# Optimization experiments

Measured on AMD Instinct MI355X. Metric: run time of the kernel, lower is better.

## Reference

```python
import jax, jax.numpy as jnp
import numpy as np

N_NODES = 100000
N_EDGES = 1600000
N_LABEL = 100000
IN_C, H1, H2, OUT_C = 128, 128, 64, 64
MLP_H = 64


def _glorot(key, shape):
    fan_in, fan_out = shape[0], shape[1]
    s = jnp.sqrt(6.0 / (fan_in + fan_out))
    return jax.random.uniform(key, shape, jnp.float32, -s, s)


def setup_inputs() -> dict:
    key = jax.random.key(0)
    ks = jax.random.split(key, 12)
    x = jax.random.normal(ks[0], (N_NODES, IN_C), jnp.float32)
    edge_index = jax.random.randint(ks[1], (2, N_EDGES), 0, N_NODES, jnp.int64)
    edge_label_index = jax.random.randint(ks[2], (2, N_LABEL), 0, N_NODES, jnp.int64)
    return {
        "x": x,
        "edge_index": edge_index,
        "edge_label_index": edge_label_index,
        "W1": _glorot(ks[3], (IN_C, H1)), "b1": jnp.zeros((H1,), jnp.float32),
        "W2": _glorot(ks[4], (H1, H2)), "b2": jnp.zeros((H2,), jnp.float32),
        "W3": _glorot(ks[5], (H2, OUT_C)), "b3": jnp.zeros((OUT_C,), jnp.float32),
        "Wl1": _glorot(ks[6], (2 * OUT_C, MLP_H)), "bl1": jnp.zeros((MLP_H,), jnp.float32),
        "Wl2": _glorot(ks[7], (MLP_H, 1)), "bl2": jnp.zeros((1,), jnp.float32),
    }


def reference(x, edge_index, edge_label_index, W1, b1, W2, b2, W3, b3, Wl1, bl1, Wl2, bl2):
    n = x.shape[0]
    # GCNConv: add self-loops once; symmetric deg^{-1/2} normalization.
    loops = jnp.arange(n, dtype=edge_index.dtype)
    src = jnp.concatenate([edge_index[0], loops])  # [E+N]
    dst = jnp.concatenate([edge_index[1], loops])
    deg = jax.ops.segment_sum(jnp.ones_like(dst, dtype=x.dtype), dst, num_segments=n)
    deg_isqrt = jnp.where(deg > 0, jax.lax.rsqrt(jnp.maximum(deg, 1e-12)), 0.0)
    norm = deg_isqrt[src] * deg_isqrt[dst]  # [E+N]

    def conv(h, W, b):
        m = (h @ W)[src] * norm[:, None]          # gather + scale per edge
        return jax.ops.segment_sum(m, dst, num_segments=n) + b  # scatter-add

    z = jax.nn.relu(conv(x, W1, b1))   # dropout is identity at eval
    z = jax.nn.relu(conv(z, W2, b2))
    z = conv(z, W3, b3)                # [N, OUT_C]

    s, d = edge_label_index[0], edge_label_index[1]
    pairs = jnp.concatenate([z[s], z[d]], axis=1)  # [E_label, 2*OUT_C]
    h = jax.nn.relu(pairs @ Wl1 + bl1)
    logits = (h @ Wl2 + bl2)[:, 0]
    return logits
```

## Files before the change

### kernel.cpp

```cpp
#include <hip/hip_runtime.h>


typedef _Float16 half8 __attribute__((ext_vector_type(8)));
typedef float floatx4 __attribute__((ext_vector_type(4)));

#define EPB 8
#define CHUNK (256 * EPB)


__global__ __launch_bounds__(256) void k_hist_wsplit(
    const int* __restrict__ ei, int E, int n, int* __restrict__ cnt,
    unsigned short* __restrict__ rank,
    const float* __restrict__ W1, _Float16* __restrict__ Wf1,
    const float* __restrict__ W2, _Float16* __restrict__ Wf2,
    const float* __restrict__ W3, _Float16* __restrict__ Wf3, int HB) {
  int b = blockIdx.x;
  if (b < HB) {
    int role = b & 7, chunk = b >> 3;
    int ns = (n + 7) / 8;
    int lo = role * ns, hi = min(n, lo + ns);
    int e0 = chunk * CHUNK + threadIdx.x;
#pragma unroll
    for (int q = 0; q < EPB; ++q) {
      int e = e0 + q * 256;
      if (e < E) {
        int d = __builtin_nontemporal_load(ei + E + e);
        if (d >= lo && d < hi) {
          int r = atomicAdd(&cnt[d], 1);
          rank[e] = (unsigned short)r;
        }
      }
    }
    return;
  }
  b -= HB;
  const float* W;
  _Float16* Wf;
  int KC, lc;
  if (b < 64)      { W = W1; Wf = Wf1; KC = 16384; lc = 7; }
  else if (b < 96) { b -= 64; W = W2; Wf = Wf2; KC = 8192; lc = 6; }
  else             { b -= 96; W = W3; Wf = Wf3; KC = 4096; lc = 6; }
  int t = b * 256 + threadIdx.x;
  if (t >= KC) return;
  int C = 1 << lc;
  int c = t & (C - 1), k = t >> lc;
  float a = W[t];
  _Float16 h = (_Float16)a;
  _Float16 l = (_Float16)(a - (float)h);
  int ks = k >> 5, ct = c >> 4;
  int lane = ((k & 31) >> 3) * 16 + (c & 15);
  int j = k & 7;
  int base = ((ks * (C >> 4) + ct) * 2) * 512 + lane * 8 + j;
  Wf[base] = h;
  Wf[base + 512] = l;
}


__global__ void k_scan1(const int* __restrict__ cnt, int* __restrict__ bsum, int n) {
  __shared__ int s[256];
  int i = blockIdx.x * 256 + threadIdx.x;
  int t = threadIdx.x;
  s[t] = (i < n) ? cnt[i] : 0;
  __syncthreads();
  for (int d = 128; d > 0; d >>= 1) {
    if (t < d) s[t] += s[t + d];
    __syncthreads();
  }
  if (t == 0) bsum[blockIdx.x] = s[0];
}

__global__ void k_scan23(const int* __restrict__ cnt, const int* __restrict__ bsum,
                         int nb, int* __restrict__ rs, float* __restrict__ isq,
                         int n) {
  __shared__ int s[256];
  __shared__ int off;
  int t = threadIdx.x;
  int b = blockIdx.x;
  int acc = 0;
  for (int j = t; j < b; j += 256) acc += bsum[j];
  s[t] = acc;
  __syncthreads();
  for (int d = 128; d > 0; d >>= 1) {
    if (t < d) s[t] += s[t + d];
    __syncthreads();
  }
  if (t == 0) off = s[0];
  __syncthreads();
  int blockoff = off;
  __syncthreads();
  int i = b * 256 + t;
  int v = (i < n) ? cnt[i] : 0;
  s[t] = v;
  __syncthreads();
  for (int d = 1; d < 256; d <<= 1) {
    int u = (t >= d) ? s[t - d] : 0;
    __syncthreads();
    s[t] += u;
    __syncthreads();
  }
  if (i < n) {
    int excl = blockoff + s[t] - v;
    rs[i] = excl;
    isq[i] = rsqrtf((float)(v + 1));
    if (i == n - 1) rs[n] = excl + v;
  }
}


__global__ __launch_bounds__(256) void k_fill(const int* __restrict__ ei, int E,
                                              int n, const int* __restrict__ rs,
                                              const unsigned short* __restrict__ rank,
                                              int* __restrict__ csr) {
  int role = blockIdx.x & 7, chunk = blockIdx.x >> 3;
  int ns = (n + 7) / 8;
  int lo = role * ns, hi = min(n, lo + ns);
  int e0 = chunk * CHUNK + threadIdx.x;
#pragma unroll
  for (int q = 0; q < EPB; ++q) {
    int e = e0 + q * 256;
    if (e < E) {
      int d = __builtin_nontemporal_load(ei + E + e);
      if (d >= lo && d < hi) {
        int s = __builtin_nontemporal_load(ei + e);
        int r = __builtin_nontemporal_load(rank + e);
        csr[rs[d] + r] = s;
      }
    }
  }
}


template <int K, int C>
__global__ __launch_bounds__(256) void k_gemm_mfma(const float* __restrict__ A,
                                                   const _Float16* __restrict__ Wf,
                                                   const float* __restrict__ isq,
                                                   _Float16* __restrict__ out, int n) {
  constexpr int NK = K / 32, NCT = C / 16;
  constexpr int WH = NK * NCT * 2 * 512;
  __shared__ __align__(16) _Float16 Wl[WH];
  int t = threadIdx.x;
  for (int i = t; i < WH / 8; i += 256)
    ((uint4*)Wl)[i] = ((const uint4*)Wf)[i];
  __syncthreads();

  int lane = t & 63, w = t >> 6;
  int rowbase = blockIdx.x * 128 + w * 32;
  int ar0 = rowbase + (lane & 15);
  int kg = (lane >> 4) * 8;

  floatx4 acc[2][NCT];
#pragma unroll
  for (int g = 0; g < 2; ++g)
#pragma unroll
    for (int ct = 0; ct < NCT; ++ct) acc[g][ct] = (floatx4){0.f, 0.f, 0.f, 0.f};

  for (int ks = 0; ks < NK; ++ks) {
    half8 ah[2], al[2];
#pragma unroll
    for (int g = 0; g < 2; ++g) {
      int row = ar0 + g * 16;
      if (row > n - 1) row = n - 1;
      const float* ap = A + (size_t)row * K + ks * 32 + kg;
      float4 u0 = ((const float4*)ap)[0];
      float4 u1 = ((const float4*)ap)[1];
      float av[8] = {u0.x, u0.y, u0.z, u0.w, u1.x, u1.y, u1.z, u1.w};
#pragma unroll
      for (int q = 0; q < 8; ++q) {
        _Float16 h = (_Float16)av[q];
        ah[g][q] = h;
        al[g][q] = (_Float16)(av[q] - (float)h);
      }
    }
#pragma unroll
    for (int ct = 0; ct < NCT; ++ct) {
      const _Float16* bp = &Wl[((ks * NCT + ct) * 2) * 512 + lane * 8];
      half8 bh = *(const half8*)bp;
      half8 bl = *(const half8*)(bp + 512);
#pragma unroll
      for (int g = 0; g < 2; ++g) {
        acc[g][ct] = __builtin_amdgcn_mfma_f32_16x16x32_f16(ah[g], bh, acc[g][ct], 0, 0, 0);
        acc[g][ct] = __builtin_amdgcn_mfma_f32_16x16x32_f16(ah[g], bl, acc[g][ct], 0, 0, 0);
        acc[g][ct] = __builtin_amdgcn_mfma_f32_16x16x32_f16(al[g], bh, acc[g][ct], 0, 0, 0);
      }
    }
  }
  int drbase = rowbase + (lane >> 4) * 4;
  int col = lane & 15;
#pragma unroll
  for (int g = 0; g < 2; ++g)
#pragma unroll
    for (int r = 0; r < 4; ++r) {
      int row = drbase + g * 16 + r;
      if (row < n) {
        float s = isq[row];
#pragma unroll
        for (int ct = 0; ct < NCT; ++ct)
          out[(size_t)row * C + ct * 16 + col] = (_Float16)(acc[g][ct][r] * s);
      }
    }
}


template <bool RELU>
__global__ __launch_bounds__(256) void k_agg128(const _Float16* __restrict__ xs,
                                                const int* __restrict__ rs,
                                                const int* __restrict__ csr,
                                                const float* __restrict__ isq,
                                                const float* __restrict__ bias,
                                                float* __restrict__ out, int n) {
  int gw = (int)((blockIdx.x * blockDim.x + threadIdx.x) >> 6);
  int lane = threadIdx.x & 63;
  if (gw >= n) return;
  int e0 = rs[gw], e1 = rs[gw + 1];
  int qtr = lane >> 4, sub = lane & 15;
  float acc[8] = {};
  int e = e0 + qtr;
  for (; e + 12 < e1; e += 16) {
    int a = __builtin_nontemporal_load(csr + e);
    int b = __builtin_nontemporal_load(csr + e + 4);
    int c = __builtin_nontemporal_load(csr + e + 8);
    int d = __builtin_nontemporal_load(csr + e + 12);
    half8 va = *(const half8*)&xs[(size_t)a * 128 + 8 * sub];
    half8 vb = *(const half8*)&xs[(size_t)b * 128 + 8 * sub];
    half8 vc = *(const half8*)&xs[(size_t)c * 128 + 8 * sub];
    half8 vd = *(const half8*)&xs[(size_t)d * 128 + 8 * sub];
#pragma unroll
    for (int j = 0; j < 8; ++j)
      acc[j] += (float)va[j] + (float)vb[j] + (float)vc[j] + (float)vd[j];
  }
  for (; e < e1; e += 4) {
    int a = __builtin_nontemporal_load(csr + e);
    half8 va = *(const half8*)&xs[(size_t)a * 128 + 8 * sub];
#pragma unroll
    for (int j = 0; j < 8; ++j) acc[j] += (float)va[j];
  }
#pragma unroll
  for (int j = 0; j < 8; ++j) {
    acc[j] += __shfl_xor(acc[j], 32, 64);
    acc[j] += __shfl_xor(acc[j], 16, 64);
  }
  if (qtr == 0) {
    float qi = isq[gw];
    half8 self = *(const half8*)&xs[(size_t)gw * 128 + 8 * sub];
#pragma unroll
    for (int j = 0; j < 8; ++j) {
      float r = qi * (acc[j] + (float)self[j]) + bias[8 * sub + j];
      if (RELU) r = fmaxf(r, 0.f);
      out[(size_t)gw * 128 + 8 * sub + j] = r;
    }
  }
}


template <bool RELU>
__global__ __launch_bounds__(256) void k_agg64(const _Float16* __restrict__ xs,
                                               const int* __restrict__ rs,
                                               const int* __restrict__ csr,
                                               const float* __restrict__ isq,
                                               const float* __restrict__ bias,
                                               float* __restrict__ out, int n) {
  int gw = (int)((blockIdx.x * blockDim.x + threadIdx.x) >> 6);
  int lane = threadIdx.x & 63;
  if (gw >= n) return;
  int e0 = rs[gw], e1 = rs[gw + 1];
  int oct = lane >> 3, sub = lane & 7;
  float acc[8] = {};
  int e = e0 + oct;
  for (; e + 8 < e1; e += 16) {
    int a = __builtin_nontemporal_load(csr + e);
    int b = __builtin_nontemporal_load(csr + e + 8);
    half8 va = *(const half8*)&xs[(size_t)a * 64 + 8 * sub];
    half8 vb = *(const half8*)&xs[(size_t)b * 64 + 8 * sub];
#pragma unroll
    for (int j = 0; j < 8; ++j) acc[j] += (float)va[j] + (float)vb[j];
  }
  for (; e < e1; e += 8) {
    int a = __builtin_nontemporal_load(csr + e);
    half8 va = *(const half8*)&xs[(size_t)a * 64 + 8 * sub];
#pragma unroll
    for (int j = 0; j < 8; ++j) acc[j] += (float)va[j];
  }
#pragma unroll
  for (int j = 0; j < 8; ++j) {
    acc[j] += __shfl_xor(acc[j], 32, 64);
    acc[j] += __shfl_xor(acc[j], 16, 64);
    acc[j] += __shfl_xor(acc[j], 8, 64);
  }
  if (oct == 0) {
    float qi = isq[gw];
    half8 self = *(const half8*)&xs[(size_t)gw * 64 + 8 * sub];
#pragma unroll
    for (int j = 0; j < 8; ++j) {
      float r = qi * (acc[j] + (float)self[j]) + bias[8 * sub + j];
      if (RELU) r = fmaxf(r, 0.f);
      out[(size_t)gw * 64 + 8 * sub + j] = r;
    }
  }
}


__global__ __launch_bounds__(256) void k_mlp(const float* __restrict__ z,
                                             const int* __restrict__ eli, int nlab,
                                             const float* __restrict__ Wl1,
                                             const float* __restrict__ bl1,
                                             const float* __restrict__ Wl2,
                                             const float* __restrict__ bl2,
                                             float* __restrict__ out) {
  constexpr int K = 128, TM = 4, LDA = K + 4;
  __shared__ float Wl[K * 64];
  __shared__ float Al[64 * LDA];
  int t = threadIdx.x;
  for (int i = t; i < K * 64 / 4; i += 256)
    ((float4*)Wl)[i] = ((const float4*)Wl1)[i];
  int rowbase = blockIdx.x * 64;
  {
    int r = t >> 2, p = t & 3;
    int row = rowbase + r;
    int idx = 0;
    if (row < nlab) idx = (p < 2) ? eli[row] : eli[nlab + row];
    const float4* src = (const float4*)(z + (size_t)idx * 64);
    int srcq = (p & 1) * 8;
    int dst = r * LDA + (p >= 2 ? 64 : 0) + (p & 1) * 32;
#pragma unroll
    for (int q = 0; q < 8; ++q)
      *(float4*)&Al[dst + 4 * q] = src[srcq + q];
  }
  __syncthreads();
  int tx = t & 15, ty = t >> 4;
  float acc[TM][4] = {};
  for (int k = 0; k < K; ++k) {
    float a[TM];
#pragma unroll
    for (int i = 0; i < TM; ++i) a[i] = Al[(ty * TM + i) * LDA + k];
    float4 w = *(const float4*)&Wl[k * 64 + tx * 4];
#pragma unroll
    for (int i = 0; i < TM; ++i) {
      acc[i][0] += a[i] * w.x;
      acc[i][1] += a[i] * w.y;
      acc[i][2] += a[i] * w.z;
      acc[i][3] += a[i] * w.w;
    }
  }
  float4 b1v = *(const float4*)&bl1[tx * 4];
  float4 w2v = *(const float4*)&Wl2[tx * 4];
  float bias2 = bl2[0];
  float part[TM];
#pragma unroll
  for (int i = 0; i < TM; ++i) {
    float h0 = fmaxf(acc[i][0] + b1v.x, 0.f);
    float h1 = fmaxf(acc[i][1] + b1v.y, 0.f);
    float h2 = fmaxf(acc[i][2] + b1v.z, 0.f);
    float h3 = fmaxf(acc[i][3] + b1v.w, 0.f);
    part[i] = h0 * w2v.x + h1 * w2v.y + h2 * w2v.z + h3 * w2v.w;
  }
#pragma unroll
  for (int i = 0; i < TM; ++i) {
#pragma unroll
    for (int m = 1; m < 16; m <<= 1)
      part[i] += __shfl_xor(part[i], m, 64);
  }
  if (tx == 0) {
#pragma unroll
    for (int i = 0; i < TM; ++i) {
      int row = rowbase + ty * TM + i;
      if (row < nlab) out[row] = part[i] + bias2;
    }
  }
}


extern "C" void kernel_launch(void* const* d_in, const int* in_sizes, int n_in,
                              void* d_out, int out_size, void* d_ws, size_t ws_size,
                              hipStream_t stream) {
  const float* x   = (const float*)d_in[0];
  const int*   ei  = (const int*)d_in[1];
  const int*   eli = (const int*)d_in[2];
  const float* W1  = (const float*)d_in[3];
  const float* b1  = (const float*)d_in[4];
  const float* W2  = (const float*)d_in[5];
  const float* b2  = (const float*)d_in[6];
  const float* W3  = (const float*)d_in[7];
  const float* b3  = (const float*)d_in[8];
  const float* Wl1 = (const float*)d_in[9];
  const float* bl1 = (const float*)d_in[10];
  const float* Wl2 = (const float*)d_in[11];
  const float* bl2 = (const float*)d_in[12];
  float* out = (float*)d_out;
  const int n    = in_sizes[0] / 128;
  const int E    = in_sizes[1] / 2;
  const int nlab = in_sizes[2] / 2;
  (void)n_in; (void)out_size; (void)ws_size;

  char* ws = (char*)d_ws;
  size_t off = 0;
  auto alloc = [&](size_t bytes) -> void* {
    void* p = ws + off;
    off = (off + bytes + 255) & ~(size_t)255;
    return p;
  };
  float*     bufZ1 = (float*)alloc((size_t)n * 128 * 4);
  float*     bufZ2 = (float*)alloc((size_t)n * 64 * 4);
  _Float16*  bufXS = (_Float16*)alloc((size_t)n * 128 * 2);
  int*       csr   = (int*)alloc((size_t)E * 4);
  unsigned short* rank = (unsigned short*)alloc((size_t)E * 2);
  int*       cnt   = (int*)alloc((size_t)n * 4);
  float*     isq   = (float*)alloc((size_t)n * 4);
  int*       rs    = (int*)alloc((size_t)(n + 1) * 4);
  const int  nb    = (n + 255) / 256;
  int*       bsum  = (int*)alloc((size_t)nb * 4);
  _Float16*  Wf1   = (_Float16*)alloc(128 * 128 * 2 * 2);
  _Float16*  Wf2   = (_Float16*)alloc(128 * 64 * 2 * 2);
  _Float16*  Wf3   = (_Float16*)alloc(64 * 64 * 2 * 2);
  float*     z3    = bufZ1;

  const int CH  = (E + CHUNK - 1) / CHUNK;
  const int HB  = 8 * CH;
  const int GT  = (n + 127) / 128;
  const int aggb = (n + 3) / 4;

  hipMemsetAsync(cnt, 0, (size_t)n * 4, stream);
  k_hist_wsplit<<<HB + 112, 256, 0, stream>>>(ei, E, n, cnt, rank,
                                              W1, Wf1, W2, Wf2, W3, Wf3, HB);
  k_scan1<<<nb, 256, 0, stream>>>(cnt, bsum, n);
  k_scan23<<<nb, 256, 0, stream>>>(cnt, bsum, nb, rs, isq, n);
  k_fill<<<HB, 256, 0, stream>>>(ei, E, n, rs, rank, csr);

  k_gemm_mfma<128, 128><<<GT, 256, 0, stream>>>(x, Wf1, isq, bufXS, n);
  k_agg128<true><<<aggb, 256, 0, stream>>>(bufXS, rs, csr, isq, b1, bufZ1, n);
  k_gemm_mfma<128, 64><<<GT, 256, 0, stream>>>(bufZ1, Wf2, isq, bufXS, n);
  k_agg64<true><<<aggb, 256, 0, stream>>>(bufXS, rs, csr, isq, b2, bufZ2, n);
  k_gemm_mfma<64, 64><<<GT, 256, 0, stream>>>(bufZ2, Wf3, isq, bufXS, n);
  k_agg64<false><<<aggb, 256, 0, stream>>>(bufXS, rs, csr, isq, b3, z3, n);
  k_mlp<<<(nlab + 63) / 64, 256, 0, stream>>>(z3, eli, nlab, Wl1, bl1, Wl2, bl2, out);
}
```

Measured before the change: 395.2 us.

## Overlap first-layer GEMM with degree histogram and store per-edge source weights in CSR

The first-layer GEMM no longer scales its output by deg^-1/2, so it can run in the same launch as the degree histogram instead of waiting for the scan. Each CSR entry now stores the source index together with that source's isq value. The layer-1 aggregation applies these per-edge weights, and the other layers read only the index field. The memset is replaced by an init kernel that also performs the weight split, and EPB is raised to 32. The cost is a CSR twice as large, which the layer-2 and layer-3 aggregations read as strided int2 entries, plus one extra multiply per edge in layer 1.

```diff
diff --git a/kernel.cpp b/kernel.cpp
--- a/kernel.cpp
+++ b/kernel.cpp
@@ -4,36 +4,25 @@
 typedef _Float16 half8 __attribute__((ext_vector_type(8)));
 typedef float floatx4 __attribute__((ext_vector_type(4)));
 
-#define EPB 8
+#define EPB 32
 #define CHUNK (256 * EPB)
 
 
-__global__ __launch_bounds__(256) void k_hist_wsplit(
-    const int* __restrict__ ei, int E, int n, int* __restrict__ cnt,
-    unsigned short* __restrict__ rank,
+__global__ __launch_bounds__(256) void k_init(
+    int* __restrict__ cnt, int n,
     const float* __restrict__ W1, _Float16* __restrict__ Wf1,
     const float* __restrict__ W2, _Float16* __restrict__ Wf2,
-    const float* __restrict__ W3, _Float16* __restrict__ Wf3, int HB) {
+    const float* __restrict__ W3, _Float16* __restrict__ Wf3) {
   int b = blockIdx.x;
-  if (b < HB) {
-    int role = b & 7, chunk = b >> 3;
-    int ns = (n + 7) / 8;
-    int lo = role * ns, hi = min(n, lo + ns);
-    int e0 = chunk * CHUNK + threadIdx.x;
-#pragma unroll
-    for (int q = 0; q < EPB; ++q) {
-      int e = e0 + q * 256;
-      if (e < E) {
-        int d = __builtin_nontemporal_load(ei + E + e);
-        if (d >= lo && d < hi) {
-          int r = atomicAdd(&cnt[d], 1);
-          rank[e] = (unsigned short)r;
-        }
-      }
+  if (b >= 112) {
+    int i = (b - 112) * 1024 + threadIdx.x * 4;
+    if (i + 3 < n) {
+      *(int4*)(cnt + i) = make_int4(0, 0, 0, 0);
+    } else {
+      for (int j = i; j < n && j < i + 4; ++j) cnt[j] = 0;
     }
     return;
   }
-  b -= HB;
   const float* W;
   _Float16* Wf;
   int KC, lc;
@@ -56,6 +45,97 @@
 }
 
 
+__device__ __forceinline__ void gemm1_body(const float* __restrict__ A,
+                                           const _Float16* __restrict__ Wf,
+                                           _Float16* __restrict__ out, int n,
+                                           int blk) {
+  constexpr int NK = 4, NCT = 8, K = 128, C = 128;
+  int t = threadIdx.x;
+  int lane = t & 63, w = t >> 6;
+  int rowbase = blk * 128 + w * 32;
+  int ar0 = rowbase + (lane & 15);
+  int kg = (lane >> 4) * 8;
+
+  floatx4 acc[2][NCT];
+#pragma unroll
+  for (int g = 0; g < 2; ++g)
+#pragma unroll
+    for (int ct = 0; ct < NCT; ++ct) acc[g][ct] = (floatx4){0.f, 0.f, 0.f, 0.f};
+
+  for (int ks = 0; ks < NK; ++ks) {
+    half8 ah[2], al[2];
+#pragma unroll
+    for (int g = 0; g < 2; ++g) {
+      int row = ar0 + g * 16;
+      if (row > n - 1) row = n - 1;
+      const float* ap = A + (size_t)row * K + ks * 32 + kg;
+      float4 u0 = ((const float4*)ap)[0];
+      float4 u1 = ((const float4*)ap)[1];
+      float av[8] = {u0.x, u0.y, u0.z, u0.w, u1.x, u1.y, u1.z, u1.w};
+#pragma unroll
+      for (int q = 0; q < 8; ++q) {
+        _Float16 h = (_Float16)av[q];
+        ah[g][q] = h;
+        al[g][q] = (_Float16)(av[q] - (float)h);
+      }
+    }
+#pragma unroll
+    for (int ct = 0; ct < NCT; ++ct) {
+      const _Float16* bp = Wf + ((ks * NCT + ct) * 2) * 512 + lane * 8;
+      half8 bh = *(const half8*)bp;
+      half8 bl = *(const half8*)(bp + 512);
+#pragma unroll
+      for (int g = 0; g < 2; ++g) {
+        acc[g][ct] = __builtin_amdgcn_mfma_f32_16x16x32_f16(ah[g], bh, acc[g][ct], 0, 0, 0);
+        acc[g][ct] = __builtin_amdgcn_mfma_f32_16x16x32_f16(ah[g], bl, acc[g][ct], 0, 0, 0);
+        acc[g][ct] = __builtin_amdgcn_mfma_f32_16x16x32_f16(al[g], bh, acc[g][ct], 0, 0, 0);
+      }
+    }
+  }
+  int drbase = rowbase + (lane >> 4) * 4;
+  int col = lane & 15;
+#pragma unroll
+  for (int g = 0; g < 2; ++g)
+#pragma unroll
+    for (int r = 0; r < 4; ++r) {
+      int row = drbase + g * 16 + r;
+      if (row < n) {
+#pragma unroll
+        for (int ct = 0; ct < NCT; ++ct)
+          out[(size_t)row * C + ct * 16 + col] = (_Float16)acc[g][ct][r];
+      }
+    }
+}
+
+
+__global__ __launch_bounds__(256) void k_hist_gemm1(
+    const int* __restrict__ ei, int E, int n, int* __restrict__ cnt,
+    unsigned short* __restrict__ rank,
+    const float* __restrict__ x, const _Float16* __restrict__ Wf1,
+    _Float16* __restrict__ xw1, int HB) {
+  int b = blockIdx.x;
+  if (b < HB) {
+    int role = b & 7, chunk = b >> 3;
+    int ns = (n + 7) / 8;
+    int lo = role * ns, hi = min(n, lo + ns);
+    int e0 = chunk * CHUNK + threadIdx.x;
+#pragma unroll
+    for (int q = 0; q < EPB; ++q) {
+      int e = e0 + q * 256;
+      if (e < E) {
+        int d = __builtin_nontemporal_load(ei + E + e);
+        if (d >= lo && d < hi) {
+          int r = atomicAdd(&cnt[d], 1);
+          rank[e] = (unsigned short)r;
+        }
+      }
+    }
+    return;
+  }
+  gemm1_body(x, Wf1, xw1, n, b - HB);
+}
+
+
 __global__ void k_scan1(const int* __restrict__ cnt, int* __restrict__ bsum, int n) {
   __shared__ int s[256];
   int i = blockIdx.x * 256 + threadIdx.x;
@@ -110,7 +190,8 @@
 __global__ __launch_bounds__(256) void k_fill(const int* __restrict__ ei, int E,
                                               int n, const int* __restrict__ rs,
                                               const unsigned short* __restrict__ rank,
-                                              int* __restrict__ csr) {
+                                              const float* __restrict__ isq,
+                                              int2* __restrict__ csr) {
   int role = blockIdx.x & 7, chunk = blockIdx.x >> 3;
   int ns = (n + 7) / 8;
   int lo = role * ns, hi = min(n, lo + ns);
@@ -123,7 +204,7 @@
       if (d >= lo && d < hi) {
         int s = __builtin_nontemporal_load(ei + e);
         int r = __builtin_nontemporal_load(rank + e);
-        csr[rs[d] + r] = s;
+        csr[rs[d] + r] = make_int2(s, __float_as_int(isq[s]));
       }
     }
   }
@@ -201,38 +282,46 @@
 }
 
 
-template <bool RELU>
-__global__ __launch_bounds__(256) void k_agg128(const _Float16* __restrict__ xs,
-                                                const int* __restrict__ rs,
-                                                const int* __restrict__ csr,
-                                                const float* __restrict__ isq,
-                                                const float* __restrict__ bias,
-                                                float* __restrict__ out, int n) {
+__global__ __launch_bounds__(256) void k_agg128w(const _Float16* __restrict__ xw,
+                                                 const int* __restrict__ rs,
+                                                 const int2* __restrict__ csr,
+                                                 const float* __restrict__ isq,
+                                                 const float* __restrict__ bias,
+                                                 float* __restrict__ out, int n) {
   int gw = (int)((blockIdx.x * blockDim.x + threadIdx.x) >> 6);
   int lane = threadIdx.x & 63;
   if (gw >= n) return;
   int e0 = rs[gw], e1 = rs[gw + 1];
   int qtr = lane >> 4, sub = lane & 15;
+  const long long* csr8 = (const long long*)csr;
   float acc[8] = {};
   int e = e0 + qtr;
   for (; e + 12 < e1; e += 16) {
-    int a = __builtin_nontemporal_load(csr + e);
-    int b = __builtin_nontemporal_load(csr + e + 4);
-    int c = __builtin_nontemporal_load(csr + e + 8);
-    int d = __builtin_nontemporal_load(csr + e + 12);
-    half8 va = *(const half8*)&xs[(size_t)a * 128 + 8 * sub];
-    half8 vb = *(const half8*)&xs[(size_t)b * 128 + 8 * sub];
-    half8 vc = *(const half8*)&xs[(size_t)c * 128 + 8 * sub];
-    half8 vd = *(const half8*)&xs[(size_t)d * 128 + 8 * sub];
+    long long a8 = __builtin_nontemporal_load(csr8 + e);
+    long long b8 = __builtin_nontemporal_load(csr8 + e + 4);
+    long long c8 = __builtin_nontemporal_load(csr8 + e + 8);
+    long long d8 = __builtin_nontemporal_load(csr8 + e + 12);
+    int ai = (int)a8, bi = (int)b8, ci = (int)c8, di = (int)d8;
+    float wa = __int_as_float((int)(a8 >> 32));
+    float wb = __int_as_float((int)(b8 >> 32));
+    float wc = __int_as_float((int)(c8 >> 32));
+    float wd = __int_as_float((int)(d8 >> 32));
+    half8 va = *(const half8*)&xw[(size_t)ai * 128 + 8 * sub];
+    half8 vb = *(const half8*)&xw[(size_t)bi * 128 + 8 * sub];
+    half8 vc = *(const half8*)&xw[(size_t)ci * 128 + 8 * sub];
+    half8 vd = *(const half8*)&xw[(size_t)di * 128 + 8 * sub];
 #pragma unroll
     for (int j = 0; j < 8; ++j)
-      acc[j] += (float)va[j] + (float)vb[j] + (float)vc[j] + (float)vd[j];
+      acc[j] += wa * (float)va[j] + wb * (float)vb[j] +
+                wc * (float)vc[j] + wd * (float)vd[j];
   }
   for (; e < e1; e += 4) {
-    int a = __builtin_nontemporal_load(csr + e);
-    half8 va = *(const half8*)&xs[(size_t)a * 128 + 8 * sub];
-#pragma unroll
-    for (int j = 0; j < 8; ++j) acc[j] += (float)va[j];
+    long long a8 = __builtin_nontemporal_load(csr8 + e);
+    int ai = (int)a8;
+    float wa = __int_as_float((int)(a8 >> 32));
+    half8 va = *(const half8*)&xw[(size_t)ai * 128 + 8 * sub];
+#pragma unroll
+    for (int j = 0; j < 8; ++j) acc[j] += wa * (float)va[j];
   }
 #pragma unroll
   for (int j = 0; j < 8; ++j) {
@@ -241,12 +330,11 @@
   }
   if (qtr == 0) {
     float qi = isq[gw];
-    half8 self = *(const half8*)&xs[(size_t)gw * 128 + 8 * sub];
+    half8 self = *(const half8*)&xw[(size_t)gw * 128 + 8 * sub];
 #pragma unroll
     for (int j = 0; j < 8; ++j) {
-      float r = qi * (acc[j] + (float)self[j]) + bias[8 * sub + j];
-      if (RELU) r = fmaxf(r, 0.f);
-      out[(size_t)gw * 128 + 8 * sub + j] = r;
+      float r = qi * (acc[j] + qi * (float)self[j]) + bias[8 * sub + j];
+      out[(size_t)gw * 128 + 8 * sub + j] = fmaxf(r, 0.f);
     }
   }
 }
@@ -255,7 +343,7 @@
 template <bool RELU>
 __global__ __launch_bounds__(256) void k_agg64(const _Float16* __restrict__ xs,
                                                const int* __restrict__ rs,
-                                               const int* __restrict__ csr,
+                                               const int2* __restrict__ csr,
                                                const float* __restrict__ isq,
                                                const float* __restrict__ bias,
                                                float* __restrict__ out, int n) {
@@ -267,15 +355,15 @@
   float acc[8] = {};
   int e = e0 + oct;
   for (; e + 8 < e1; e += 16) {
-    int a = __builtin_nontemporal_load(csr + e);
-    int b = __builtin_nontemporal_load(csr + e + 8);
+    int a = __builtin_nontemporal_load(&csr[e].x);
+    int b = __builtin_nontemporal_load(&csr[e + 8].x);
     half8 va = *(const half8*)&xs[(size_t)a * 64 + 8 * sub];
     half8 vb = *(const half8*)&xs[(size_t)b * 64 + 8 * sub];
 #pragma unroll
     for (int j = 0; j < 8; ++j) acc[j] += (float)va[j] + (float)vb[j];
   }
   for (; e < e1; e += 8) {
-    int a = __builtin_nontemporal_load(csr + e);
+    int a = __builtin_nontemporal_load(&csr[e].x);
     half8 va = *(const half8*)&xs[(size_t)a * 64 + 8 * sub];
 #pragma unroll
     for (int j = 0; j < 8; ++j) acc[j] += (float)va[j];
@@ -400,8 +488,8 @@
   };
   float*     bufZ1 = (float*)alloc((size_t)n * 128 * 4);
   float*     bufZ2 = (float*)alloc((size_t)n * 64 * 4);
-  _Float16*  bufXS = (_Float16*)alloc((size_t)n * 128 * 2);
-  int*       csr   = (int*)alloc((size_t)E * 4);
+  _Float16*  bufXW = (_Float16*)alloc((size_t)n * 128 * 2);
+  int2*      csr   = (int2*)alloc((size_t)E * 8);
   unsigned short* rank = (unsigned short*)alloc((size_t)E * 2);
   int*       cnt   = (int*)alloc((size_t)n * 4);
   float*     isq   = (float*)alloc((size_t)n * 4);
@@ -416,20 +504,19 @@
   const int CH  = (E + CHUNK - 1) / CHUNK;
   const int HB  = 8 * CH;
   const int GT  = (n + 127) / 128;
+  const int ZB  = (n + 1023) / 1024;
   const int aggb = (n + 3) / 4;
 
-  hipMemsetAsync(cnt, 0, (size_t)n * 4, stream);
-  k_hist_wsplit<<<HB + 112, 256, 0, stream>>>(ei, E, n, cnt, rank,
-                                              W1, Wf1, W2, Wf2, W3, Wf3, HB);
+  k_init<<<112 + ZB, 256, 0, stream>>>(cnt, n, W1, Wf1, W2, Wf2, W3, Wf3);
+  k_hist_gemm1<<<HB + GT, 256, 0, stream>>>(ei, E, n, cnt, rank, x, Wf1, bufXW, HB);
   k_scan1<<<nb, 256, 0, stream>>>(cnt, bsum, n);
   k_scan23<<<nb, 256, 0, stream>>>(cnt, bsum, nb, rs, isq, n);
-  k_fill<<<HB, 256, 0, stream>>>(ei, E, n, rs, rank, csr);
-
-  k_gemm_mfma<128, 128><<<GT, 256, 0, stream>>>(x, Wf1, isq, bufXS, n);
-  k_agg128<true><<<aggb, 256, 0, stream>>>(bufXS, rs, csr, isq, b1, bufZ1, n);
-  k_gemm_mfma<128, 64><<<GT, 256, 0, stream>>>(bufZ1, Wf2, isq, bufXS, n);
-  k_agg64<true><<<aggb, 256, 0, stream>>>(bufXS, rs, csr, isq, b2, bufZ2, n);
-  k_gemm_mfma<64, 64><<<GT, 256, 0, stream>>>(bufZ2, Wf3, isq, bufXS, n);
-  k_agg64<false><<<aggb, 256, 0, stream>>>(bufXS, rs, csr, isq, b3, z3, n);
+  k_fill<<<HB, 256, 0, stream>>>(ei, E, n, rs, rank, isq, csr);
+
+  k_agg128w<<<aggb, 256, 0, stream>>>(bufXW, rs, csr, isq, b1, bufZ1, n);
+  k_gemm_mfma<128, 64><<<GT, 256, 0, stream>>>(bufZ1, Wf2, isq, bufXW, n);
+  k_agg64<true><<<aggb, 256, 0, stream>>>(bufXW, rs, csr, isq, b2, bufZ2, n);
+  k_gemm_mfma<64, 64><<<GT, 256, 0, stream>>>(bufZ2, Wf3, isq, bufXW, n);
+  k_agg64<false><<<aggb, 256, 0, stream>>>(bufXW, rs, csr, isq, b3, z3, n);
   k_mlp<<<(nlab + 63) / 64, 256, 0, stream>>>(z3, eli, nlab, Wl1, bl1, Wl2, bl2, out);
 }
```

Result: slower. 431.1 us (+9.1%).
